# Kernel optimization log

Hardware: AMD Instinct MI355X
Metric: run time of the kernel (lower is better)

The kernel has to match this reference:

```python
import jax, jax.numpy as jnp
import numpy as np

N = 8192          # number of nodes
DIN = 512         # in_features
DOUT = 256        # out_features
P_EDGE = 0.004    # ~32 avg degree
NEG_INF = -9e15   # matches the torch module's -9000000000000000.0 mask value


def setup_inputs() -> dict:
    key = jax.random.key(0)
    ks = jax.random.split(key, 7)
    x = jax.random.normal(ks[0], (N, DIN), dtype=jnp.float32)
    # binary adjacency, Bernoulli(P_EDGE)
    adj = (jax.random.uniform(ks[1], (N, N)) < P_EDGE).astype(jnp.float32)
    W1 = jax.random.normal(ks[2], (DIN, DOUT), dtype=jnp.float32) * 0.05
    b1 = jnp.zeros((DOUT,), dtype=jnp.float32)
    a1_w = jax.random.normal(ks[3], (DOUT,), dtype=jnp.float32) * 0.05
    a1_b = jnp.zeros((), dtype=jnp.float32)
    a2_w = jax.random.normal(ks[4], (DOUT,), dtype=jnp.float32) * 0.05
    a2_b = jnp.zeros((), dtype=jnp.float32)
    return {"x": x, "adj": adj, "W1": W1, "b1": b1,
            "a1_w": a1_w, "a1_b": a1_b, "a2_w": a2_w, "a2_b": a2_b}


def reference(x, adj, W1, b1, a1_w, a1_b, a2_w, a2_b):
    # h = linear1(elu(x))                       [n, DOUT]
    h = jnp.matmul(jax.nn.elu(x), W1) + b1
    # per-node scalar scores g1 (source/col) and g2 (dest/row)
    g1 = h @ a1_w + a1_b                       # [n]
    g2 = h @ a2_w + a2_b                       # [n]
    # kron trick collapses to: scores[i,j] = adj[i,j] * (g2[i] + g1[j])
    scores = adj * (g2[:, None] + g1[None, :])  # [n, n]
    e = jax.nn.leaky_relu(scores, negative_slope=0.2)
    attention = jax.nn.softmax(jnp.where(adj > 0, e, NEG_INF), axis=1)
    # untied=False path: weighted aggregation of h (dropout p=0 is identity)
    return attention @ h
```

## Files before the change

### kernel.cpp

```cpp
#include <hip/hip_runtime.h>
#include <hip/hip_bf16.h>
#include <cstdint>
#include <cstddef>

#define N_NODES 8192
#define DIN 512
#define DOUT 256
#define CAP 512

typedef short bf16x8 __attribute__((ext_vector_type(8)));
typedef float f32x4 __attribute__((ext_vector_type(4)));
typedef unsigned int u32x4 __attribute__((ext_vector_type(4)));

__device__ __forceinline__ float bf2f(unsigned short u) {
    union { unsigned int ui; float f; } v; v.ui = ((unsigned int)u) << 16; return v.f;
}
__device__ __forceinline__ unsigned short f2bf(float f) {
    union { float f; unsigned int u; } v; v.f = f;
    unsigned int u = v.u;
    return (unsigned short)((u + 0x7fffu + ((u >> 16) & 1u)) >> 16);
}
__device__ __forceinline__ float elu1(float v) { return v > 0.f ? v : (expf(v) - 1.f); }

__global__ __launch_bounds__(256) void gemm_h_kernel(
    const float* __restrict__ x, const float* __restrict__ W1,
    const float* __restrict__ b1, unsigned short* __restrict__ h)
{
    const int tid = threadIdx.x;
    const int wave = tid >> 6, lane = tid & 63;
    const int quad = lane >> 4, r16 = lane & 15;
    const int m0 = (blockIdx.x >> 2) * 64;
    const int col = (blockIdx.x & 3) * 64 + wave * 16 + r16;

    f32x4 acc[4] = {{0.f,0.f,0.f,0.f},{0.f,0.f,0.f,0.f},{0.f,0.f,0.f,0.f},{0.f,0.f,0.f,0.f}};

    for (int k0 = 0; k0 < DIN; k0 += 32) {
        const int kbase = k0 + quad * 8;
        bf16x8 bfr;
        #pragma unroll
        for (int j = 0; j < 8; ++j)
            bfr[j] = (short)f2bf(W1[(size_t)(kbase + j) * DOUT + col]);
        #pragma unroll
        for (int r = 0; r < 4; ++r) {
            const float* xrow = x + (size_t)(m0 + r * 16 + r16) * DIN;
            float4 f0 = *(const float4*)(xrow + kbase);
            float4 f1 = *(const float4*)(xrow + kbase + 4);
            bf16x8 af;
            af[0] = (short)f2bf(elu1(f0.x)); af[1] = (short)f2bf(elu1(f0.y));
            af[2] = (short)f2bf(elu1(f0.z)); af[3] = (short)f2bf(elu1(f0.w));
            af[4] = (short)f2bf(elu1(f1.x)); af[5] = (short)f2bf(elu1(f1.y));
            af[6] = (short)f2bf(elu1(f1.z)); af[7] = (short)f2bf(elu1(f1.w));
            acc[r] = __builtin_amdgcn_mfma_f32_16x16x32_bf16(af, bfr, acc[r], 0, 0, 0);
        }
    }
    const float bias = b1[col];
    #pragma unroll
    for (int r = 0; r < 4; ++r)
        #pragma unroll
        for (int rr = 0; rr < 4; ++rr)
            h[(size_t)(m0 + r * 16 + quad * 4 + rr) * DOUT + col] = f2bf(acc[r][rr] + bias);
}

__global__ __launch_bounds__(256) void g12_kernel(
    const unsigned short* __restrict__ h,
    const float* __restrict__ a1w, const float* __restrict__ a1b,
    const float* __restrict__ a2w, const float* __restrict__ a2b,
    float* __restrict__ g1, float* __restrict__ g2)
{
    const int tid = threadIdx.x;
    const int wave = tid >> 6, lane = tid & 63;
    const int i = blockIdx.x * 4 + wave;
    const int d0 = lane * 4;
    ushort4 hv = *(const ushort4*)(h + (size_t)i * DOUT + d0);
    float4 w1 = *(const float4*)(a1w + d0);
    float4 w2 = *(const float4*)(a2w + d0);
    float h0 = bf2f(hv.x), h1 = bf2f(hv.y), h2 = bf2f(hv.z), h3 = bf2f(hv.w);
    float s1 = h0*w1.x + h1*w1.y + h2*w1.z + h3*w1.w;
    float s2 = h0*w2.x + h1*w2.y + h2*w2.z + h3*w2.w;
    #pragma unroll
    for (int off = 32; off > 0; off >>= 1) {
        s1 += __shfl_xor(s1, off, 64);
        s2 += __shfl_xor(s2, off, 64);
    }
    if (lane == 0) {
        g1[i] = s1 + a1b[0];
        g2[i] = s2 + a2b[0];
    }
}

__global__ __launch_bounds__(256) void agg_kernel(
    const float* __restrict__ adj, const unsigned short* __restrict__ h,
    const float* __restrict__ g1, const float* __restrict__ g2,
    float* __restrict__ out)
{
    __shared__ int   eidx[CAP];
    __shared__ float ev[CAP];
    __shared__ float red[256];
    __shared__ int   cnt;

    const int tid = threadIdx.x;
    const int i = blockIdx.x;
    if (tid == 0) cnt = 0;
    __syncthreads();

    const float g2i = g2[i];
    const float* arow = adj + (size_t)i * N_NODES;

    u32x4 raws[8];
    #pragma unroll
    for (int c = 0; c < 8; ++c)
        raws[c] = __builtin_nontemporal_load((const u32x4*)(arow + c * 1024 + tid * 4));

    #pragma unroll
    for (int c = 0; c < 8; ++c) {
        u32x4 raw = raws[c];
        if (raw.x | raw.y | raw.z | raw.w) {
            unsigned int wv[4] = {raw.x, raw.y, raw.z, raw.w};
            #pragma unroll
            for (int q = 0; q < 4; ++q) {
                if (wv[q]) {
                    int j = c * 1024 + tid * 4 + q;
                    union { unsigned int u; float f; } av; av.u = wv[q];
                    float s = av.f * (g2i + g1[j]);
                    float lr = s > 0.f ? s : 0.2f * s;
                    int pos = atomicAdd(&cnt, 1);
                    if (pos < CAP) { eidx[pos] = j; ev[pos] = lr; }
                }
            }
        }
    }
    __syncthreads();
    const int K = cnt < CAP ? cnt : CAP;

    if (K == 0) {
        float acc = 0.f;
        for (int j = 0; j < N_NODES; ++j) acc += bf2f(h[(size_t)j * DOUT + tid]);
        out[(size_t)i * DOUT + tid] = acc / (float)N_NODES;
        return;
    }

    float mloc = -1e30f;
    for (int k = tid; k < K; k += 256) mloc = fmaxf(mloc, ev[k]);
    red[tid] = mloc; __syncthreads();
    for (int s = 128; s > 0; s >>= 1) {
        if (tid < s) red[tid] = fmaxf(red[tid], red[tid + s]);
        __syncthreads();
    }
    const float m = red[0];
    __syncthreads();

    float sloc = 0.f;
    for (int k = tid; k < K; k += 256) { float p = expf(ev[k] - m); ev[k] = p; sloc += p; }
    red[tid] = sloc; __syncthreads();
    for (int s = 128; s > 0; s >>= 1) {
        if (tid < s) red[tid] += red[tid + s];
        __syncthreads();
    }
    const float inv = 1.f / red[0];

    float acc = 0.f;
    int k = 0;
    for (; k + 4 <= K; k += 4) {
        float p0 = ev[k],     p1 = ev[k + 1], p2 = ev[k + 2], p3 = ev[k + 3];
        int   j0 = eidx[k],   j1 = eidx[k+1], j2 = eidx[k+2], j3 = eidx[k+3];
        float v0 = bf2f(h[(size_t)j0 * DOUT + tid]);
        float v1 = bf2f(h[(size_t)j1 * DOUT + tid]);
        float v2 = bf2f(h[(size_t)j2 * DOUT + tid]);
        float v3 = bf2f(h[(size_t)j3 * DOUT + tid]);
        acc += p0 * v0 + p1 * v1 + p2 * v2 + p3 * v3;
    }
    for (; k < K; ++k) acc += ev[k] * bf2f(h[(size_t)eidx[k] * DOUT + tid]);
    out[(size_t)i * DOUT + tid] = acc * inv;
}

extern "C" void kernel_launch(void* const* d_in, const int* in_sizes, int n_in,
                              void* d_out, int out_size, void* d_ws, size_t ws_size,
                              hipStream_t stream) {
    const float* x   = (const float*)d_in[0];
    const float* adj = (const float*)d_in[1];
    const float* W1  = (const float*)d_in[2];
    const float* b1  = (const float*)d_in[3];
    const float* a1w = (const float*)d_in[4];
    const float* a1b = (const float*)d_in[5];
    const float* a2w = (const float*)d_in[6];
    const float* a2b = (const float*)d_in[7];

    float* g1 = (float*)d_ws;
    float* g2 = g1 + N_NODES;
    unsigned short* h = (unsigned short*)(g2 + N_NODES);
    float* out = (float*)d_out;

    hipLaunchKernelGGL(gemm_h_kernel, dim3(512),  dim3(256), 0, stream, x, W1, b1, h);
    hipLaunchKernelGGL(g12_kernel,    dim3(2048), dim3(256), 0, stream, h, a1w, a1b, a2w, a2b, g1, g2);
    hipLaunchKernelGGL(agg_kernel,    dim3(8192), dim3(256), 0, stream, adj, h, g1, g2, out);
}
```

Measured before the change: 424.0 us.

## Split aggregation into adjacency-scan and softmax-gather kernels via workspace edge lists

The fused aggregation kernel is split in two. A scan kernel streams each adjacency row and writes the compacted neighbour indices and leaky-relu scores to global workspace. A separate finish kernel reloads them, computes the softmax with a single-wave shuffle reduction instead of block-wide shared-memory tree reductions, and gathers h. The intent is to separate the bandwidth-bound scan from the latency-bound gather and cut sync overhead. The cost is an extra launch plus a workspace write and read of up to 32 MB.

```diff
diff --git a/kernel.cpp b/kernel.cpp
--- a/kernel.cpp
+++ b/kernel.cpp
@@ -88,14 +88,13 @@
     }
 }
 
-__global__ __launch_bounds__(256) void agg_kernel(
-    const float* __restrict__ adj, const unsigned short* __restrict__ h,
-    const float* __restrict__ g1, const float* __restrict__ g2,
-    float* __restrict__ out)
+__global__ __launch_bounds__(256) void scan_kernel(
+    const float* __restrict__ adj, const float* __restrict__ g1,
+    const float* __restrict__ g2,
+    int* __restrict__ ej, float* __restrict__ evg, int* __restrict__ cnts)
 {
     __shared__ int   eidx[CAP];
     __shared__ float ev[CAP];
-    __shared__ float red[256];
     __shared__ int   cnt;
 
     const int tid = threadIdx.x;
@@ -131,6 +130,25 @@
     }
     __syncthreads();
     const int K = cnt < CAP ? cnt : CAP;
+    for (int k = tid; k < K; k += 256) {
+        ej[(size_t)i * CAP + k]  = eidx[k];
+        evg[(size_t)i * CAP + k] = ev[k];
+    }
+    if (tid == 0) cnts[i] = K;
+}
+
+__global__ __launch_bounds__(256) void finish_kernel(
+    const int* __restrict__ ej, const float* __restrict__ evg,
+    const int* __restrict__ cnts, const unsigned short* __restrict__ h,
+    float* __restrict__ out)
+{
+    __shared__ int   jbuf[CAP];
+    __shared__ float pbuf[CAP];
+    __shared__ float sinv;
+
+    const int tid = threadIdx.x;
+    const int i = blockIdx.x;
+    const int K = cnts[i];
 
     if (K == 0) {
         float acc = 0.f;
@@ -139,37 +157,39 @@
         return;
     }
 
-    float mloc = -1e30f;
-    for (int k = tid; k < K; k += 256) mloc = fmaxf(mloc, ev[k]);
-    red[tid] = mloc; __syncthreads();
-    for (int s = 128; s > 0; s >>= 1) {
-        if (tid < s) red[tid] = fmaxf(red[tid], red[tid + s]);
-        __syncthreads();
-    }
-    const float m = red[0];
-    __syncthreads();
-
-    float sloc = 0.f;
-    for (int k = tid; k < K; k += 256) { float p = expf(ev[k] - m); ev[k] = p; sloc += p; }
-    red[tid] = sloc; __syncthreads();
-    for (int s = 128; s > 0; s >>= 1) {
-        if (tid < s) red[tid] += red[tid + s];
-        __syncthreads();
-    }
-    const float inv = 1.f / red[0];
+    for (int k = tid; k < K; k += 256) {
+        jbuf[k] = ej[(size_t)i * CAP + k];
+        pbuf[k] = evg[(size_t)i * CAP + k];
+    }
+    __syncthreads();
+
+    if (tid < 64) {
+        const int lane = tid;
+        float mloc = -1e30f;
+        for (int k = lane; k < K; k += 64) mloc = fmaxf(mloc, pbuf[k]);
+        #pragma unroll
+        for (int off = 32; off > 0; off >>= 1) mloc = fmaxf(mloc, __shfl_xor(mloc, off, 64));
+        float sloc = 0.f;
+        for (int k = lane; k < K; k += 64) { float p = expf(pbuf[k] - mloc); pbuf[k] = p; sloc += p; }
+        #pragma unroll
+        for (int off = 32; off > 0; off >>= 1) sloc += __shfl_xor(sloc, off, 64);
+        if (lane == 0) sinv = 1.f / sloc;
+    }
+    __syncthreads();
+    const float inv = sinv;
 
     float acc = 0.f;
     int k = 0;
     for (; k + 4 <= K; k += 4) {
-        float p0 = ev[k],     p1 = ev[k + 1], p2 = ev[k + 2], p3 = ev[k + 3];
-        int   j0 = eidx[k],   j1 = eidx[k+1], j2 = eidx[k+2], j3 = eidx[k+3];
+        float p0 = pbuf[k],   p1 = pbuf[k+1], p2 = pbuf[k+2], p3 = pbuf[k+3];
+        int   j0 = jbuf[k],   j1 = jbuf[k+1], j2 = jbuf[k+2], j3 = jbuf[k+3];
         float v0 = bf2f(h[(size_t)j0 * DOUT + tid]);
         float v1 = bf2f(h[(size_t)j1 * DOUT + tid]);
         float v2 = bf2f(h[(size_t)j2 * DOUT + tid]);
         float v3 = bf2f(h[(size_t)j3 * DOUT + tid]);
         acc += p0 * v0 + p1 * v1 + p2 * v2 + p3 * v3;
     }
-    for (; k < K; ++k) acc += ev[k] * bf2f(h[(size_t)eidx[k] * DOUT + tid]);
+    for (; k < K; ++k) acc += pbuf[k] * bf2f(h[(size_t)jbuf[k] * DOUT + tid]);
     out[(size_t)i * DOUT + tid] = acc * inv;
 }
 
@@ -185,12 +205,17 @@
     const float* a2w = (const float*)d_in[6];
     const float* a2b = (const float*)d_in[7];
 
-    float* g1 = (float*)d_ws;
-    float* g2 = g1 + N_NODES;
-    unsigned short* h = (unsigned short*)(g2 + N_NODES);
+    char* w = (char*)d_ws;
+    float* g1 = (float*)w;                                   w += (size_t)N_NODES * 4;
+    float* g2 = (float*)w;                                   w += (size_t)N_NODES * 4;
+    unsigned short* h = (unsigned short*)w;                  w += (size_t)N_NODES * DOUT * 2;
+    int* ej = (int*)w;                                       w += (size_t)N_NODES * CAP * 4;
+    float* evg = (float*)w;                                  w += (size_t)N_NODES * CAP * 4;
+    int* cnts = (int*)w;
     float* out = (float*)d_out;
 
-    hipLaunchKernelGGL(gemm_h_kernel, dim3(512),  dim3(256), 0, stream, x, W1, b1, h);
-    hipLaunchKernelGGL(g12_kernel,    dim3(2048), dim3(256), 0, stream, h, a1w, a1b, a2w, a2b, g1, g2);
-    hipLaunchKernelGGL(agg_kernel,    dim3(8192), dim3(256), 0, stream, adj, h, g1, g2, out);
-}
+    hipLaunchKernelGGL(gemm_h_kernel,  dim3(512),  dim3(256), 0, stream, x, W1, b1, h);
+    hipLaunchKernelGGL(g12_kernel,     dim3(2048), dim3(256), 0, stream, h, a1w, a1b, a2w, a2b, g1, g2);
+    hipLaunchKernelGGL(scan_kernel,    dim3(8192), dim3(256), 0, stream, adj, g1, g2, ej, evg, cnts);
+    hipLaunchKernelGGL(finish_kernel,  dim3(8192), dim3(256), 0, stream, ej, evg, cnts, h, out);
+}
```

Measured after the change: 427.0 us. Within noise of the previous version (+0.7%).

## Map one wavefront per row in aggregation with ballot-based edge compaction

Applied to the files above, without the earlier changes.

The aggregation kernel now gives each 64-lane wave its own row, so a block covers four rows. Edges are compacted with ballot and mbcnt prefix counts instead of a shared atomic counter, and the softmax reductions use wave shuffles instead of block-wide shared-memory trees with barriers. Each lane now gathers four bf16 features per h row with vector loads. This removes the block barriers and LDS atomics, but each wave now streams a whole 32KB adjacency row alone, and the nontemporal load hint is dropped.

```diff
diff --git a/kernel.cpp b/kernel.cpp
--- a/kernel.cpp
+++ b/kernel.cpp
@@ -21,6 +21,10 @@
     return (unsigned short)((u + 0x7fffu + ((u >> 16) & 1u)) >> 16);
 }
 __device__ __forceinline__ float elu1(float v) { return v > 0.f ? v : (expf(v) - 1.f); }
+__device__ __forceinline__ int mbcnt64(unsigned long long m) {
+    return __builtin_amdgcn_mbcnt_hi((unsigned)(m >> 32),
+           __builtin_amdgcn_mbcnt_lo((unsigned)m, 0));
+}
 
 __global__ __launch_bounds__(256) void gemm_h_kernel(
     const float* __restrict__ x, const float* __restrict__ W1,
@@ -88,89 +92,95 @@
     }
 }
 
-__global__ __launch_bounds__(256) void agg_kernel(
+__global__ __launch_bounds__(256, 4) void agg_kernel(
     const float* __restrict__ adj, const unsigned short* __restrict__ h,
     const float* __restrict__ g1, const float* __restrict__ g2,
     float* __restrict__ out)
 {
-    __shared__ int   eidx[CAP];
-    __shared__ float ev[CAP];
-    __shared__ float red[256];
-    __shared__ int   cnt;
+    __shared__ int   eidx_s[4][CAP];
+    __shared__ float ev_s[4][CAP];
 
     const int tid = threadIdx.x;
-    const int i = blockIdx.x;
-    if (tid == 0) cnt = 0;
-    __syncthreads();
+    const int wave = tid >> 6, lane = tid & 63;
+    const int i = blockIdx.x * 4 + wave;
+    int*   my_ei = eidx_s[wave];
+    float* my_ev = ev_s[wave];
 
     const float g2i = g2[i];
     const float* arow = adj + (size_t)i * N_NODES;
 
-    u32x4 raws[8];
-    #pragma unroll
-    for (int c = 0; c < 8; ++c)
-        raws[c] = __builtin_nontemporal_load((const u32x4*)(arow + c * 1024 + tid * 4));
-
-    #pragma unroll
-    for (int c = 0; c < 8; ++c) {
-        u32x4 raw = raws[c];
-        if (raw.x | raw.y | raw.z | raw.w) {
-            unsigned int wv[4] = {raw.x, raw.y, raw.z, raw.w};
+    int base = 0;
+    for (int cc = 0; cc < 4; ++cc) {
+        u32x4 raws[8];
+        #pragma unroll
+        for (int c = 0; c < 8; ++c)
+            raws[c] = *(const u32x4*)(arow + (cc * 8 + c) * 256 + lane * 4);
+        #pragma unroll
+        for (int c = 0; c < 8; ++c) {
+            const int jb = (cc * 8 + c) * 256 + lane * 4;
+            unsigned int wv[4] = {raws[c].x, raws[c].y, raws[c].z, raws[c].w};
             #pragma unroll
             for (int q = 0; q < 4; ++q) {
-                if (wv[q]) {
-                    int j = c * 1024 + tid * 4 + q;
-                    union { unsigned int u; float f; } av; av.u = wv[q];
-                    float s = av.f * (g2i + g1[j]);
-                    float lr = s > 0.f ? s : 0.2f * s;
-                    int pos = atomicAdd(&cnt, 1);
-                    if (pos < CAP) { eidx[pos] = j; ev[pos] = lr; }
+                bool nz = wv[q] != 0u;
+                unsigned long long mask = __ballot(nz);
+                if (mask) {
+                    if (nz) {
+                        int pos = base + mbcnt64(mask);
+                        if (pos < CAP) {
+                            int j = jb + q;
+                            union { unsigned int u; float f; } av; av.u = wv[q];
+                            float s = av.f * (g2i + g1[j]);
+                            my_ei[pos] = j;
+                            my_ev[pos] = s > 0.f ? s : 0.2f * s;
+                        }
+                    }
+                    base += __popcll(mask);
                 }
             }
         }
     }
-    __syncthreads();
-    const int K = cnt < CAP ? cnt : CAP;
+    const int K = base < CAP ? base : CAP;
 
     if (K == 0) {
-        float acc = 0.f;
-        for (int j = 0; j < N_NODES; ++j) acc += bf2f(h[(size_t)j * DOUT + tid]);
-        out[(size_t)i * DOUT + tid] = acc / (float)N_NODES;
+        float a0 = 0.f, a1 = 0.f, a2 = 0.f, a3 = 0.f;
+        for (int j = 0; j < N_NODES; ++j) {
+            ushort4 hv = *(const ushort4*)(h + (size_t)j * DOUT + lane * 4);
+            a0 += bf2f(hv.x); a1 += bf2f(hv.y); a2 += bf2f(hv.z); a3 += bf2f(hv.w);
+        }
+        float4 o = {a0 / N_NODES, a1 / N_NODES, a2 / N_NODES, a3 / N_NODES};
+        *(float4*)(out + (size_t)i * DOUT + lane * 4) = o;
         return;
     }
 
     float mloc = -1e30f;
-    for (int k = tid; k < K; k += 256) mloc = fmaxf(mloc, ev[k]);
-    red[tid] = mloc; __syncthreads();
-    for (int s = 128; s > 0; s >>= 1) {
-        if (tid < s) red[tid] = fmaxf(red[tid], red[tid + s]);
-        __syncthreads();
-    }
-    const float m = red[0];
-    __syncthreads();
-
+    for (int k = lane; k < K; k += 64) mloc = fmaxf(mloc, my_ev[k]);
+    #pragma unroll
+    for (int off = 32; off > 0; off >>= 1) mloc = fmaxf(mloc, __shfl_xor(mloc, off, 64));
     float sloc = 0.f;
-    for (int k = tid; k < K; k += 256) { float p = expf(ev[k] - m); ev[k] = p; sloc += p; }
-    red[tid] = sloc; __syncthreads();
-    for (int s = 128; s > 0; s >>= 1) {
-        if (tid < s) red[tid] += red[tid + s];
-        __syncthreads();
-    }
-    const float inv = 1.f / red[0];
-
-    float acc = 0.f;
+    for (int k = lane; k < K; k += 64) { float p = expf(my_ev[k] - mloc); my_ev[k] = p; sloc += p; }
+    #pragma unroll
+    for (int off = 32; off > 0; off >>= 1) sloc += __shfl_xor(sloc, off, 64);
+    const float inv = 1.f / sloc;
+
+    float a0 = 0.f, a1 = 0.f, a2 = 0.f, a3 = 0.f;
     int k = 0;
     for (; k + 4 <= K; k += 4) {
-        float p0 = ev[k],     p1 = ev[k + 1], p2 = ev[k + 2], p3 = ev[k + 3];
-        int   j0 = eidx[k],   j1 = eidx[k+1], j2 = eidx[k+2], j3 = eidx[k+3];
-        float v0 = bf2f(h[(size_t)j0 * DOUT + tid]);
-        float v1 = bf2f(h[(size_t)j1 * DOUT + tid]);
-        float v2 = bf2f(h[(size_t)j2 * DOUT + tid]);
-        float v3 = bf2f(h[(size_t)j3 * DOUT + tid]);
-        acc += p0 * v0 + p1 * v1 + p2 * v2 + p3 * v3;
-    }
-    for (; k < K; ++k) acc += ev[k] * bf2f(h[(size_t)eidx[k] * DOUT + tid]);
-    out[(size_t)i * DOUT + tid] = acc * inv;
+        #pragma unroll
+        for (int u = 0; u < 4; ++u) {
+            int jj = my_ei[k + u]; float p = my_ev[k + u];
+            ushort4 hv = *(const ushort4*)(h + (size_t)jj * DOUT + lane * 4);
+            a0 += p * bf2f(hv.x); a1 += p * bf2f(hv.y);
+            a2 += p * bf2f(hv.z); a3 += p * bf2f(hv.w);
+        }
+    }
+    for (; k < K; ++k) {
+        int jj = my_ei[k]; float p = my_ev[k];
+        ushort4 hv = *(const ushort4*)(h + (size_t)jj * DOUT + lane * 4);
+        a0 += p * bf2f(hv.x); a1 += p * bf2f(hv.y);
+        a2 += p * bf2f(hv.z); a3 += p * bf2f(hv.w);
+    }
+    float4 o = {a0 * inv, a1 * inv, a2 * inv, a3 * inv};
+    *(float4*)(out + (size_t)i * DOUT + lane * 4) = o;
 }
 
 extern "C" void kernel_launch(void* const* d_in, const int* in_sizes, int n_in,
@@ -192,5 +202,5 @@
 
     hipLaunchKernelGGL(gemm_h_kernel, dim3(512),  dim3(256), 0, stream, x, W1, b1, h);
     hipLaunchKernelGGL(g12_kernel,    dim3(2048), dim3(256), 0, stream, h, a1w, a1b, a2w, a2b, g1, g2);
-    hipLaunchKernelGGL(agg_kernel,    dim3(8192), dim3(256), 0, stream, adj, h, g1, g2, out);
-}
+    hipLaunchKernelGGL(agg_kernel,    dim3(2048), dim3(256), 0, stream, adj, h, g1, g2, out);
+}
```

Result: slower. 439.4 us (+3.6%).

## Pre-convert x and W1 to bf16 and use larger register-tiled GEMM

Applied to the files above, without the earlier changes.

Adds separate kernels that apply ELU and convert x to bf16 once, and that transpose and convert W1 to bf16 in a K-contiguous layout. The GEMM then loads packed bf16 vectors directly and computes a 64x64 tile per wave with 16 MFMA accumulators, rather than redoing the ELU and conversion per tile and gathering W1 with strided scalar loads. The trade-off is two extra launches and extra workspace traffic. The GEMM grid also shrinks to 128 blocks, which may underfill the GPU. The aggregation kernel, likely the dominant cost, is unchanged.

```diff
diff --git a/kernel.cpp b/kernel.cpp
--- a/kernel.cpp
+++ b/kernel.cpp
@@ -11,6 +11,7 @@
 typedef short bf16x8 __attribute__((ext_vector_type(8)));
 typedef float f32x4 __attribute__((ext_vector_type(4)));
 typedef unsigned int u32x4 __attribute__((ext_vector_type(4)));
+typedef unsigned short u16x8 __attribute__((ext_vector_type(8)));
 
 __device__ __forceinline__ float bf2f(unsigned short u) {
     union { unsigned int ui; float f; } v; v.ui = ((unsigned int)u) << 16; return v.f;
@@ -22,43 +23,72 @@
 }
 __device__ __forceinline__ float elu1(float v) { return v > 0.f ? v : (expf(v) - 1.f); }
 
+__global__ __launch_bounds__(256) void convx_kernel(
+    const float* __restrict__ x, unsigned short* __restrict__ xb)
+{
+    const int idx = (blockIdx.x * 256 + threadIdx.x) * 8;
+    float4 f0 = *(const float4*)(x + idx);
+    float4 f1 = *(const float4*)(x + idx + 4);
+    u16x8 o;
+    o[0] = f2bf(elu1(f0.x)); o[1] = f2bf(elu1(f0.y));
+    o[2] = f2bf(elu1(f0.z)); o[3] = f2bf(elu1(f0.w));
+    o[4] = f2bf(elu1(f1.x)); o[5] = f2bf(elu1(f1.y));
+    o[6] = f2bf(elu1(f1.z)); o[7] = f2bf(elu1(f1.w));
+    *(u16x8*)(xb + idx) = o;
+}
+
+__global__ __launch_bounds__(256) void convw_kernel(
+    const float* __restrict__ W1, unsigned short* __restrict__ wb)
+{
+    const int n = blockIdx.x;
+    const int k = threadIdx.x * 2;
+    unsigned short a = f2bf(W1[(size_t)k * DOUT + n]);
+    unsigned short b = f2bf(W1[(size_t)(k + 1) * DOUT + n]);
+    *(unsigned int*)(wb + (size_t)n * DIN + k) = (unsigned int)a | ((unsigned int)b << 16);
+}
+
 __global__ __launch_bounds__(256) void gemm_h_kernel(
-    const float* __restrict__ x, const float* __restrict__ W1,
+    const unsigned short* __restrict__ xb, const unsigned short* __restrict__ wb,
     const float* __restrict__ b1, unsigned short* __restrict__ h)
 {
     const int tid = threadIdx.x;
     const int wave = tid >> 6, lane = tid & 63;
     const int quad = lane >> 4, r16 = lane & 15;
-    const int m0 = (blockIdx.x >> 2) * 64;
-    const int col = (blockIdx.x & 3) * 64 + wave * 16 + r16;
-
-    f32x4 acc[4] = {{0.f,0.f,0.f,0.f},{0.f,0.f,0.f,0.f},{0.f,0.f,0.f,0.f},{0.f,0.f,0.f,0.f}};
+    const int m0 = blockIdx.x * 64;
+    const int n0 = wave * 64;
+
+    f32x4 acc[4][4];
+    #pragma unroll
+    for (int mi = 0; mi < 4; ++mi)
+        #pragma unroll
+        for (int ni = 0; ni < 4; ++ni)
+            acc[mi][ni] = (f32x4){0.f, 0.f, 0.f, 0.f};
 
     for (int k0 = 0; k0 < DIN; k0 += 32) {
-        const int kbase = k0 + quad * 8;
-        bf16x8 bfr;
-        #pragma unroll
-        for (int j = 0; j < 8; ++j)
-            bfr[j] = (short)f2bf(W1[(size_t)(kbase + j) * DOUT + col]);
-        #pragma unroll
-        for (int r = 0; r < 4; ++r) {
-            const float* xrow = x + (size_t)(m0 + r * 16 + r16) * DIN;
-            float4 f0 = *(const float4*)(xrow + kbase);
-            float4 f1 = *(const float4*)(xrow + kbase + 4);
-            bf16x8 af;
-            af[0] = (short)f2bf(elu1(f0.x)); af[1] = (short)f2bf(elu1(f0.y));
-            af[2] = (short)f2bf(elu1(f0.z)); af[3] = (short)f2bf(elu1(f0.w));
-            af[4] = (short)f2bf(elu1(f1.x)); af[5] = (short)f2bf(elu1(f1.y));
-            af[6] = (short)f2bf(elu1(f1.z)); af[7] = (short)f2bf(elu1(f1.w));
-            acc[r] = __builtin_amdgcn_mfma_f32_16x16x32_bf16(af, bfr, acc[r], 0, 0, 0);
-        }
-    }
-    const float bias = b1[col];
-    #pragma unroll
-    for (int r = 0; r < 4; ++r)
-        #pragma unroll
-        for (int rr = 0; rr < 4; ++rr)
-            h[(size_t)(m0 + r * 16 + quad * 4 + rr) * DOUT + col] = f2bf(acc[r][rr] + bias);
+        const int kb = k0 + quad * 8;
+        bf16x8 A[4], B[4];
+        #pragma unroll
+        for (int s = 0; s < 4; ++s)
+            A[s] = *(const bf16x8*)(xb + (size_t)(m0 + s * 16 + r16) * DIN + kb);
+        #pragma unroll
+        for (int s = 0; s < 4; ++s)
+            B[s] = *(const bf16x8*)(wb + (size_t)(n0 + s * 16 + r16) * DIN + kb);
+        #pragma unroll
+        for (int mi = 0; mi < 4; ++mi)
+            #pragma unroll
+            for (int ni = 0; ni < 4; ++ni)
+                acc[mi][ni] = __builtin_amdgcn_mfma_f32_16x16x32_bf16(A[mi], B[ni], acc[mi][ni], 0, 0, 0);
+    }
+    #pragma unroll
+    for (int ni = 0; ni < 4; ++ni) {
+        const int col = n0 + ni * 16 + r16;
+        const float bias = b1[col];
+        #pragma unroll
+        for (int mi = 0; mi < 4; ++mi)
+            #pragma unroll
+            for (int rr = 0; rr < 4; ++rr)
+                h[(size_t)(m0 + mi * 16 + quad * 4 + rr) * DOUT + col] = f2bf(acc[mi][ni][rr] + bias);
+    }
 }
 
 __global__ __launch_bounds__(256) void g12_kernel(
@@ -185,12 +215,17 @@
     const float* a2w = (const float*)d_in[6];
     const float* a2b = (const float*)d_in[7];
 
-    float* g1 = (float*)d_ws;
-    float* g2 = g1 + N_NODES;
-    unsigned short* h = (unsigned short*)(g2 + N_NODES);
+    char* w = (char*)d_ws;
+    float* g1 = (float*)w;                     w += (size_t)N_NODES * 4;
+    float* g2 = (float*)w;                     w += (size_t)N_NODES * 4;
+    unsigned short* h  = (unsigned short*)w;   w += (size_t)N_NODES * DOUT * 2;
+    unsigned short* xb = (unsigned short*)w;   w += (size_t)N_NODES * DIN * 2;
+    unsigned short* wb = (unsigned short*)w;
     float* out = (float*)d_out;
 
-    hipLaunchKernelGGL(gemm_h_kernel, dim3(512),  dim3(256), 0, stream, x, W1, b1, h);
+    hipLaunchKernelGGL(convx_kernel,  dim3(2048), dim3(256), 0, stream, x, xb);
+    hipLaunchKernelGGL(convw_kernel,  dim3(256),  dim3(256), 0, stream, W1, wb);
+    hipLaunchKernelGGL(gemm_h_kernel, dim3(128),  dim3(256), 0, stream, xb, wb, b1, h);
     hipLaunchKernelGGL(g12_kernel,    dim3(2048), dim3(256), 0, stream, h, a1w, a1b, a2w, a2b, g1, g2);
     hipLaunchKernelGGL(agg_kernel,    dim3(8192), dim3(256), 0, stream, adj, h, g1, g2, out);
 }
```

Measured after the change: 402.1 us. 5.2% less time.
